# Optimization experiments

Hardware: AMD Instinct MI355X
Metric: run time of the kernel (lower is better)

## Reference

```python
import jax, jax.numpy as jnp
import numpy as np

B, T, K = 128, 2048, 96  # batch, seq_len, num_tags


def setup_inputs() -> dict:
    key = jax.random.key(0)
    k1, k2, k3, k4, k5 = jax.random.split(key, 5)
    logits = jax.random.normal(k1, (B, T, K), dtype=jnp.float32)
    labels = jax.random.randint(k2, (B, T), 0, K)
    mask = jnp.ones((B, T), dtype=bool)
    # learned CRF parameters
    transitions = jax.random.normal(k3, (K, K), dtype=jnp.float32) * 0.1
    start_transitions = jax.random.normal(k4, (K,), dtype=jnp.float32) * 0.1
    end_transitions = jax.random.normal(k5, (K,), dtype=jnp.float32) * 0.1
    return {
        "logits": logits,
        "labels": labels,
        "mask": mask,
        "transitions": transitions,
        "start_transitions": start_transitions,
        "end_transitions": end_transitions,
    }


def _log_partition(logits, maskf, transitions, start_transitions, end_transitions):
    # forward algorithm over time via scan; logits: [B,T,K]
    em = jnp.transpose(logits, (1, 0, 2))   # [T,B,K]
    mk = jnp.transpose(maskf, (1, 0))       # [T,B]
    alpha0 = start_transitions[None, :] + em[0]  # [B,K]

    def step(alpha, x):
        emit_t, m_t = x
        # alpha[b,i] + transitions[i,j] + emit[b,j] -> logsumexp over i
        inner = alpha[:, :, None] + transitions[None, :, :] + emit_t[:, None, :]
        new = jax.nn.logsumexp(inner, axis=1)
        alpha = jnp.where(m_t[:, None] > 0, new, alpha)
        return alpha, None

    alpha, _ = jax.lax.scan(step, alpha0, (em[1:], mk[1:]))
    return jax.nn.logsumexp(alpha + end_transitions[None, :], axis=1)  # [B]


def _joint_score(logits, labels, maskf, mask, transitions, start_transitions, end_transitions):
    b = jnp.arange(logits.shape[0])
    emit = jnp.take_along_axis(logits, labels[..., None], axis=2)[..., 0]  # [B,T]
    emit_sum = jnp.sum(emit * maskf, axis=1)
    trans = transitions[labels[:, :-1], labels[:, 1:]]                     # [B,T-1]
    trans_sum = jnp.sum(trans * maskf[:, 1:], axis=1)
    seq_len = jnp.sum(mask.astype(jnp.int32), axis=1)
    last_tags = labels[b, seq_len - 1]
    return start_transitions[labels[:, 0]] + emit_sum + trans_sum + end_transitions[last_tags]


def reference(logits, labels, mask, transitions, start_transitions, end_transitions):
    maskf = mask.astype(logits.dtype)
    logZ = _log_partition(logits, maskf, transitions, start_transitions, end_transitions)
    score = _joint_score(logits, labels, maskf, mask, transitions, start_transitions, end_transitions)
    log_lik = jnp.sum(score - logZ)
    return -log_lik
```

## Files before the change

### kernel.cpp

```cpp
#include <hip/hip_runtime.h>
#include <math.h>

#define B_ 128
#define T_ 2048
#define K_ 96
#define NC 256
#define CH 8
#define WARM 8
#define GRP 16
#define SP 100
#define LOGZ_BLOCKS (8 * NC)
#define SCORE_BLOCKS 512

typedef __attribute__((ext_vector_type(8))) short short8;
typedef __attribute__((ext_vector_type(4))) float float4v;
union U8 { unsigned u[4]; short8 v; };

__device__ __forceinline__ unsigned pack_trunc(float lo, float hi) {
    return __builtin_amdgcn_perm(__builtin_bit_cast(unsigned, hi),
                                 __builtin_bit_cast(unsigned, lo), 0x07060302u);
}
__device__ __forceinline__ unsigned short bf16_rne(float x) {
    unsigned u = __builtin_bit_cast(unsigned, x);
    u += 0x7FFFu + ((u >> 16) & 1u);
    return (unsigned short)(u >> 16);
}
__device__ __forceinline__ float wave_reduce_sum(float x) {
#pragma unroll
    for (int off = 1; off < 64; off <<= 1) x += __shfl_xor(x, off, 64);
    return x;
}

__device__ __forceinline__ void crf_mfma_step(
    int k, int len, float* __restrict__ Sw, int lo, int q,
    const short8 (&Bf)[6][3], const float* (&ep)[4],
    float (&e)[24], float &acc)
{
#pragma unroll
    for (int i = 0; i < 24; ++i) e[i] = __expf(e[i]);

    float bn0 = Sw[lo * SP];
    float R = __builtin_amdgcn_rcpf(bn0);
    acc += __logf(bn0);

    short8 Af[3];
#pragma unroll
    for (int f = 0; f < 3; ++f) {
        const float4* pp = (const float4*)&Sw[lo * SP + 32 * f + 8 * q];
        float4 v0 = pp[0], v1 = pp[1];
        U8 ua;
        ua.u[0] = pack_trunc(v0.x * R, v0.y * R);
        ua.u[1] = pack_trunc(v0.z * R, v0.w * R);
        ua.u[2] = pack_trunc(v1.x * R, v1.y * R);
        ua.u[3] = pack_trunc(v1.z * R, v1.w * R);
        Af[f] = ua.v;
    }

    float4v Cv[6];
#pragma unroll
    for (int nt = 0; nt < 6; ++nt) {
        float4v cz = {0.f, 0.f, 0.f, 0.f};
        cz = __builtin_amdgcn_mfma_f32_16x16x32_bf16(Af[0], Bf[nt][0], cz, 0, 0, 0);
        cz = __builtin_amdgcn_mfma_f32_16x16x32_bf16(Af[1], Bf[nt][1], cz, 0, 0, 0);
        Cv[nt] = __builtin_amdgcn_mfma_f32_16x16x32_bf16(Af[2], Bf[nt][2], cz, 0, 0, 0);
    }

#pragma unroll
    for (int nt = 0; nt < 6; ++nt)
#pragma unroll
        for (int r = 0; r < 4; ++r)
            Sw[(4 * q + r) * SP + 16 * nt + lo] = Cv[nt][r] * e[nt * 4 + r];

    if (k + 2 <= len) {
#pragma unroll
        for (int r = 0; r < 4; ++r) {
#pragma unroll
            for (int nt = 0; nt < 6; ++nt) e[nt * 4 + r] = ep[r][16 * nt];
            ep[r] += K_;
        }
    }
}

__global__ void __launch_bounds__(64, 3) crf_fused_kernel(
    const float* __restrict__ logits, const int* __restrict__ labels,
    const float* __restrict__ trans, const float* __restrict__ startT,
    const float* __restrict__ endT, float* __restrict__ out)
{
    __shared__ __align__(16) float Sw[GRP * SP];
    const int tid = threadIdx.x;

    if (blockIdx.x >= LOGZ_BLOCKS) {
        int gid = (blockIdx.x - LOGZ_BLOCKS) * 64 + tid;
        float acc2 = 0.f;
        for (int i = gid; i < B_ * T_; i += SCORE_BLOCKS * 64) {
            int b = i >> 11, t = i & (T_ - 1);
            const int* lab = labels + (size_t)b * T_;
            int lt = lab[t];
            acc2 += logits[((size_t)b * T_ + t) * K_ + lt];
            acc2 += (t > 0) ? trans[lab[t - 1] * K_ + lt] : startT[lt];
            if (t == T_ - 1) acc2 += endT[lt];
        }
        acc2 = wave_reduce_sum(acc2);
        if (tid == 0) atomicAdd(out, -acc2);
        return;
    }

    const int lane = tid, lo = lane & 15, q = lane >> 4;
    const int W = blockIdx.x;
    const int c = W & (NC - 1);
    const int grp = W >> 8;
    const int ts = (c == 0) ? 0 : (CH * c - WARM);
    const int len = (c == 0) ? CH : ((c < NC - 1) ? (WARM + CH) : (WARM + CH - 1));

    short8 Bf[6][3];
#pragma unroll
    for (int nt = 0; nt < 6; ++nt)
#pragma unroll
        for (int kf = 0; kf < 3; ++kf) {
            U8 ub;
#pragma unroll
            for (int p = 0; p < 4; ++p) {
                int k0 = 32 * kf + 8 * q + 2 * p;
                int n = 16 * nt + lo;
                unsigned l = bf16_rne(__expf(trans[(size_t)k0 * K_ + n]));
                unsigned h = bf16_rne(__expf(trans[(size_t)(k0 + 1) * K_ + n]));
                ub.u[p] = l | (h << 16);
            }
            Bf[nt][kf] = ub.v;
        }

    if (c == 0) {
#pragma unroll
        for (int f = 0; f < 3; ++f) {
            int k0 = 32 * f + 8 * q;
            const float* p = logits + (size_t)(grp * GRP + lo) * T_ * K_ + k0;
            float4 La = *(const float4*)p, Lb2 = *(const float4*)(p + 4);
            float4 Sa = *(const float4*)(startT + k0), Sb = *(const float4*)(startT + k0 + 4);
            float4 w0 = { __expf(La.x + Sa.x), __expf(La.y + Sa.y),
                          __expf(La.z + Sa.z), __expf(La.w + Sa.w) };
            float4 w1 = { __expf(Lb2.x + Sb.x), __expf(Lb2.y + Sb.y),
                          __expf(Lb2.z + Sb.z), __expf(Lb2.w + Sb.w) };
            float4* d0 = (float4*)&Sw[lo * SP + k0];
            d0[0] = w0; d0[1] = w1;
        }
    } else {
        float4 one = {1.f, 1.f, 1.f, 1.f};
#pragma unroll
        for (int f = 0; f < 3; ++f) {
            float4* d0 = (float4*)&Sw[lo * SP + 32 * f + 8 * q];
            d0[0] = one; d0[1] = one;
        }
    }

    const float* ep[4];
#pragma unroll
    for (int r = 0; r < 4; ++r)
        ep[r] = logits + ((size_t)(grp * GRP + 4 * q + r) * T_ + (ts + 1)) * K_ + lo;
    float eO[24], eE[24];
#pragma unroll
    for (int r = 0; r < 4; ++r) {
#pragma unroll
        for (int nt = 0; nt < 6; ++nt) eO[nt * 4 + r] = ep[r][16 * nt];
        ep[r] += K_;
    }
#pragma unroll
    for (int r = 0; r < 4; ++r) {
#pragma unroll
        for (int nt = 0; nt < 6; ++nt) eE[nt * 4 + r] = ep[r][16 * nt];
        ep[r] += K_;
    }

    float acc = 0.f, Mwarm = 0.f;
    int k = 1;
    if (c != 0) {
#pragma unroll 1
        for (int n2 = 0; n2 < WARM / 2; ++n2) {
            crf_mfma_step(k, len, Sw, lo, q, Bf, ep, eO, acc); ++k;
            crf_mfma_step(k, len, Sw, lo, q, Bf, ep, eE, acc); ++k;
        }
        float mx = 0.f;
#pragma unroll
        for (int f = 0; f < 3; ++f) {
            const float4* pp = (const float4*)&Sw[lo * SP + 32 * f + 8 * q];
            float4 v0 = pp[0], v1 = pp[1];
            mx = fmaxf(mx, fmaxf(fmaxf(v0.x, v0.y), fmaxf(v0.z, v0.w)));
            mx = fmaxf(mx, fmaxf(fmaxf(v1.x, v1.y), fmaxf(v1.z, v1.w)));
        }
        mx = fmaxf(mx, __shfl_xor(mx, 16, 64));
        mx = fmaxf(mx, __shfl_xor(mx, 32, 64));
        Mwarm = __logf(mx) + acc;
    }

    const int pairs = (len - k + 1) >> 1;
#pragma unroll 1
    for (int n2 = 0; n2 < pairs; ++n2) {
        crf_mfma_step(k, len, Sw, lo, q, Bf, ep, eO, acc); ++k;
        crf_mfma_step(k, len, Sw, lo, q, Bf, ep, eE, acc); ++k;
    }
    if (k <= len) { crf_mfma_step(k, len, Sw, lo, q, Bf, ep, eO, acc); ++k; }

    float contrib;
    if (c < NC - 1) {
        float mx = 0.f;
#pragma unroll
        for (int f = 0; f < 3; ++f) {
            const float4* pp = (const float4*)&Sw[lo * SP + 32 * f + 8 * q];
            float4 v0 = pp[0], v1 = pp[1];
            mx = fmaxf(mx, fmaxf(fmaxf(v0.x, v0.y), fmaxf(v0.z, v0.w)));
            mx = fmaxf(mx, fmaxf(fmaxf(v1.x, v1.y), fmaxf(v1.z, v1.w)));
        }
        mx = fmaxf(mx, __shfl_xor(mx, 16, 64));
        mx = fmaxf(mx, __shfl_xor(mx, 32, 64));
        contrib = __logf(mx) + acc - Mwarm;
    } else {
        float xs[24];
#pragma unroll
        for (int f = 0; f < 3; ++f) {
            int k0 = 32 * f + 8 * q;
            const float4* pp = (const float4*)&Sw[lo * SP + k0];
            float4 v0 = pp[0], v1 = pp[1];
            float4 e0 = *(const float4*)(endT + k0), e1 = *(const float4*)(endT + k0 + 4);
            xs[f * 8 + 0] = __logf(v0.x) + e0.x; xs[f * 8 + 1] = __logf(v0.y) + e0.y;
            xs[f * 8 + 2] = __logf(v0.z) + e0.z; xs[f * 8 + 3] = __logf(v0.w) + e0.w;
            xs[f * 8 + 4] = __logf(v1.x) + e1.x; xs[f * 8 + 5] = __logf(v1.y) + e1.y;
            xs[f * 8 + 6] = __logf(v1.z) + e1.z; xs[f * 8 + 7] = __logf(v1.w) + e1.w;
        }
        float m2 = -1e30f;
#pragma unroll
        for (int i = 0; i < 24; ++i) m2 = fmaxf(m2, xs[i]);
        m2 = fmaxf(m2, __shfl_xor(m2, 16, 64));
        m2 = fmaxf(m2, __shfl_xor(m2, 32, 64));
        float p2 = 0.f;
#pragma unroll
        for (int i = 0; i < 24; ++i) p2 += __expf(xs[i] - m2);
        p2 += __shfl_xor(p2, 16, 64);
        p2 += __shfl_xor(p2, 32, 64);
        contrib = m2 + __logf(p2) + acc - Mwarm;
    }

    float cv = (lane < 16) ? contrib : 0.f;
    cv = wave_reduce_sum(cv);
    if (lane == 0) atomicAdd(out, cv);
}

extern "C" void kernel_launch(void* const* d_in, const int* in_sizes, int n_in,
                              void* d_out, int out_size, void* d_ws, size_t ws_size,
                              hipStream_t stream)
{
    const float* logits = (const float*)d_in[0];
    const int*   labels = (const int*)d_in[1];
    const float* trans  = (const float*)d_in[3];
    const float* startT = (const float*)d_in[4];
    const float* endT   = (const float*)d_in[5];
    float* out = (float*)d_out;

    hipMemsetAsync(out, 0, sizeof(float), stream);
    hipLaunchKernelGGL(crf_fused_kernel, dim3(LOGZ_BLOCKS + SCORE_BLOCKS),
                       dim3(64), 0, stream,
                       logits, labels, trans, startT, endT, out);
}
```

Measured before the change: 197.7 us.

## Restructure CRF step with vectorized emission loads and fewer, longer chunks

Changes the chunked forward recurrence so that each step multiplies the emission into the A operand, using exp(emit) applied to the previous state held in registers, instead of into the stored output. Emission loads become contiguous float4 reads per lane in place of strided scalar loads. Normalization now uses a lane-0 shuffle of the MFMA result rather than an LDS read. Chunk count is halved and chunk length doubled, which shrinks the warm-up overhead fraction but halves the parallelism, and the occupancy hint drops from 3 to 2 waves.

```diff
diff --git a/kernel.cpp b/kernel.cpp
--- a/kernel.cpp
+++ b/kernel.cpp
@@ -4,13 +4,13 @@
 #define B_ 128
 #define T_ 2048
 #define K_ 96
-#define NC 256
-#define CH 8
+#define NC 128
+#define CH 16
 #define WARM 8
 #define GRP 16
 #define SP 100
 #define LOGZ_BLOCKS (8 * NC)
-#define SCORE_BLOCKS 512
+#define SCORE_BLOCKS 256
 
 typedef __attribute__((ext_vector_type(8))) short short8;
 typedef __attribute__((ext_vector_type(4))) float float4v;
@@ -31,29 +31,39 @@
     return x;
 }
 
-__device__ __forceinline__ void crf_mfma_step(
+__device__ __forceinline__ void crf_step(
     int k, int len, float* __restrict__ Sw, int lo, int q,
-    const short8 (&Bf)[6][3], const float* (&ep)[4],
-    float (&e)[24], float &acc)
+    const short8 (&Bf)[6][3], const float* __restrict__ eptr,
+    float4 (&eb)[6], float4 (&cvN)[6], float &acc)
 {
-#pragma unroll
-    for (int i = 0; i < 24; ++i) e[i] = __expf(e[i]);
-
-    float bn0 = Sw[lo * SP];
-    float R = __builtin_amdgcn_rcpf(bn0);
-    acc += __logf(bn0);
+    float4 pr[6];
+#pragma unroll
+    for (int i = 0; i < 6; ++i) {
+        float4 e = eb[i], cc = cvN[i];
+        pr[i] = make_float4(cc.x * __expf(e.x), cc.y * __expf(e.y),
+                            cc.z * __expf(e.z), cc.w * __expf(e.w));
+    }
 
     short8 Af[3];
 #pragma unroll
     for (int f = 0; f < 3; ++f) {
-        const float4* pp = (const float4*)&Sw[lo * SP + 32 * f + 8 * q];
-        float4 v0 = pp[0], v1 = pp[1];
+        float4 v0 = pr[2 * f], v1 = pr[2 * f + 1];
         U8 ua;
-        ua.u[0] = pack_trunc(v0.x * R, v0.y * R);
-        ua.u[1] = pack_trunc(v0.z * R, v0.w * R);
-        ua.u[2] = pack_trunc(v1.x * R, v1.y * R);
-        ua.u[3] = pack_trunc(v1.z * R, v1.w * R);
+        ua.u[0] = pack_trunc(v0.x, v0.y);
+        ua.u[1] = pack_trunc(v0.z, v0.w);
+        ua.u[2] = pack_trunc(v1.x, v1.y);
+        ua.u[3] = pack_trunc(v1.z, v1.w);
         Af[f] = ua.v;
+    }
+
+    if (k + 2 <= len) {
+        const float* p = eptr + (size_t)(k + 1) * K_;
+        eb[0] = *(const float4*)(p);
+        eb[1] = *(const float4*)(p + 4);
+        eb[2] = *(const float4*)(p + 32);
+        eb[3] = *(const float4*)(p + 36);
+        eb[4] = *(const float4*)(p + 64);
+        eb[5] = *(const float4*)(p + 68);
     }
 
     float4v Cv[6];
@@ -65,23 +75,36 @@
         Cv[nt] = __builtin_amdgcn_mfma_f32_16x16x32_bf16(Af[2], Bf[nt][2], cz, 0, 0, 0);
     }
 
+    float c00 = __shfl(Cv[0][0], 0, 64);
+    float R = __builtin_amdgcn_rcpf(c00);
+    acc += __logf(c00);
+
 #pragma unroll
     for (int nt = 0; nt < 6; ++nt)
 #pragma unroll
         for (int r = 0; r < 4; ++r)
-            Sw[(4 * q + r) * SP + 16 * nt + lo] = Cv[nt][r] * e[nt * 4 + r];
-
-    if (k + 2 <= len) {
-#pragma unroll
-        for (int r = 0; r < 4; ++r) {
-#pragma unroll
-            for (int nt = 0; nt < 6; ++nt) e[nt * 4 + r] = ep[r][16 * nt];
-            ep[r] += K_;
-        }
-    }
-}
-
-__global__ void __launch_bounds__(64, 3) crf_fused_kernel(
+            Sw[(4 * q + r) * SP + 16 * nt + lo] = Cv[nt][r] * R;
+
+#pragma unroll
+    for (int f = 0; f < 3; ++f) {
+        cvN[2 * f]     = *(const float4*)&Sw[lo * SP + 32 * f + 8 * q];
+        cvN[2 * f + 1] = *(const float4*)&Sw[lo * SP + 32 * f + 8 * q + 4];
+    }
+}
+
+__device__ __forceinline__ float measureM(const float4 (&cvN)[6], float acc) {
+    float mx = 0.f;
+#pragma unroll
+    for (int i = 0; i < 6; ++i) {
+        float4 v = cvN[i];
+        mx = fmaxf(mx, fmaxf(fmaxf(v.x, v.y), fmaxf(v.z, v.w)));
+    }
+    mx = fmaxf(mx, __shfl_xor(mx, 16, 64));
+    mx = fmaxf(mx, __shfl_xor(mx, 32, 64));
+    return __logf(mx) + acc;
+}
+
+__global__ void __launch_bounds__(64, 2) crf_fused_kernel(
     const float* __restrict__ logits, const int* __restrict__ labels,
     const float* __restrict__ trans, const float* __restrict__ startT,
     const float* __restrict__ endT, float* __restrict__ out)
@@ -108,7 +131,7 @@
     const int lane = tid, lo = lane & 15, q = lane >> 4;
     const int W = blockIdx.x;
     const int c = W & (NC - 1);
-    const int grp = W >> 8;
+    const int grp = W >> 7;
     const int ts = (c == 0) ? 0 : (CH * c - WARM);
     const int len = (c == 0) ? CH : ((c < NC - 1) ? (WARM + CH) : (WARM + CH - 1));
 
@@ -129,45 +152,33 @@
             Bf[nt][kf] = ub.v;
         }
 
+    float4 cvN[6];
     if (c == 0) {
 #pragma unroll
         for (int f = 0; f < 3; ++f) {
             int k0 = 32 * f + 8 * q;
-            const float* p = logits + (size_t)(grp * GRP + lo) * T_ * K_ + k0;
-            float4 La = *(const float4*)p, Lb2 = *(const float4*)(p + 4);
-            float4 Sa = *(const float4*)(startT + k0), Sb = *(const float4*)(startT + k0 + 4);
-            float4 w0 = { __expf(La.x + Sa.x), __expf(La.y + Sa.y),
-                          __expf(La.z + Sa.z), __expf(La.w + Sa.w) };
-            float4 w1 = { __expf(Lb2.x + Sb.x), __expf(Lb2.y + Sb.y),
-                          __expf(Lb2.z + Sb.z), __expf(Lb2.w + Sb.w) };
-            float4* d0 = (float4*)&Sw[lo * SP + k0];
-            d0[0] = w0; d0[1] = w1;
+            float4 s0 = *(const float4*)(startT + k0);
+            float4 s1 = *(const float4*)(startT + k0 + 4);
+            cvN[2 * f]     = make_float4(__expf(s0.x), __expf(s0.y), __expf(s0.z), __expf(s0.w));
+            cvN[2 * f + 1] = make_float4(__expf(s1.x), __expf(s1.y), __expf(s1.z), __expf(s1.w));
         }
     } else {
-        float4 one = {1.f, 1.f, 1.f, 1.f};
-#pragma unroll
-        for (int f = 0; f < 3; ++f) {
-            float4* d0 = (float4*)&Sw[lo * SP + 32 * f + 8 * q];
-            d0[0] = one; d0[1] = one;
-        }
-    }
-
-    const float* ep[4];
-#pragma unroll
-    for (int r = 0; r < 4; ++r)
-        ep[r] = logits + ((size_t)(grp * GRP + 4 * q + r) * T_ + (ts + 1)) * K_ + lo;
-    float eO[24], eE[24];
-#pragma unroll
-    for (int r = 0; r < 4; ++r) {
-#pragma unroll
-        for (int nt = 0; nt < 6; ++nt) eO[nt * 4 + r] = ep[r][16 * nt];
-        ep[r] += K_;
-    }
-#pragma unroll
-    for (int r = 0; r < 4; ++r) {
-#pragma unroll
-        for (int nt = 0; nt < 6; ++nt) eE[nt * 4 + r] = ep[r][16 * nt];
-        ep[r] += K_;
+        float4 one = make_float4(1.f, 1.f, 1.f, 1.f);
+#pragma unroll
+        for (int i = 0; i < 6; ++i) cvN[i] = one;
+    }
+
+    const float* eptr = logits + ((size_t)(grp * GRP + lo) * T_ + ts) * K_ + 8 * q;
+    float4 eb0[6], eb1[6];
+    {
+        const float* p0 = eptr;
+        eb0[0] = *(const float4*)(p0);      eb0[1] = *(const float4*)(p0 + 4);
+        eb0[2] = *(const float4*)(p0 + 32); eb0[3] = *(const float4*)(p0 + 36);
+        eb0[4] = *(const float4*)(p0 + 64); eb0[5] = *(const float4*)(p0 + 68);
+        const float* p1 = eptr + K_;
+        eb1[0] = *(const float4*)(p1);      eb1[1] = *(const float4*)(p1 + 4);
+        eb1[2] = *(const float4*)(p1 + 32); eb1[3] = *(const float4*)(p1 + 36);
+        eb1[4] = *(const float4*)(p1 + 64); eb1[5] = *(const float4*)(p1 + 68);
     }
 
     float acc = 0.f, Mwarm = 0.f;
@@ -175,72 +186,59 @@
     if (c != 0) {
 #pragma unroll 1
         for (int n2 = 0; n2 < WARM / 2; ++n2) {
-            crf_mfma_step(k, len, Sw, lo, q, Bf, ep, eO, acc); ++k;
-            crf_mfma_step(k, len, Sw, lo, q, Bf, ep, eE, acc); ++k;
-        }
-        float mx = 0.f;
-#pragma unroll
-        for (int f = 0; f < 3; ++f) {
-            const float4* pp = (const float4*)&Sw[lo * SP + 32 * f + 8 * q];
-            float4 v0 = pp[0], v1 = pp[1];
-            mx = fmaxf(mx, fmaxf(fmaxf(v0.x, v0.y), fmaxf(v0.z, v0.w)));
-            mx = fmaxf(mx, fmaxf(fmaxf(v1.x, v1.y), fmaxf(v1.z, v1.w)));
-        }
-        mx = fmaxf(mx, __shfl_xor(mx, 16, 64));
-        mx = fmaxf(mx, __shfl_xor(mx, 32, 64));
-        Mwarm = __logf(mx) + acc;
+            crf_step(k, len, Sw, lo, q, Bf, eptr, eb0, cvN, acc); ++k;
+            crf_step(k, len, Sw, lo, q, Bf, eptr, eb1, cvN, acc); ++k;
+        }
+        Mwarm = measureM(cvN, acc);
     }
 
     const int pairs = (len - k + 1) >> 1;
 #pragma unroll 1
     for (int n2 = 0; n2 < pairs; ++n2) {
-        crf_mfma_step(k, len, Sw, lo, q, Bf, ep, eO, acc); ++k;
-        crf_mfma_step(k, len, Sw, lo, q, Bf, ep, eE, acc); ++k;
-    }
-    if (k <= len) { crf_mfma_step(k, len, Sw, lo, q, Bf, ep, eO, acc); ++k; }
+        crf_step(k, len, Sw, lo, q, Bf, eptr, eb0, cvN, acc); ++k;
+        crf_step(k, len, Sw, lo, q, Bf, eptr, eb1, cvN, acc); ++k;
+    }
+    if (k <= len) { crf_step(k, len, Sw, lo, q, Bf, eptr, eb0, cvN, acc); ++k; }
 
     float contrib;
     if (c < NC - 1) {
-        float mx = 0.f;
-#pragma unroll
-        for (int f = 0; f < 3; ++f) {
-            const float4* pp = (const float4*)&Sw[lo * SP + 32 * f + 8 * q];
-            float4 v0 = pp[0], v1 = pp[1];
-            mx = fmaxf(mx, fmaxf(fmaxf(v0.x, v0.y), fmaxf(v0.z, v0.w)));
-            mx = fmaxf(mx, fmaxf(fmaxf(v1.x, v1.y), fmaxf(v1.z, v1.w)));
-        }
-        mx = fmaxf(mx, __shfl_xor(mx, 16, 64));
-        mx = fmaxf(mx, __shfl_xor(mx, 32, 64));
-        contrib = __logf(mx) + acc - Mwarm;
+        contrib = measureM(cvN, acc) - Mwarm;
     } else {
-        float xs[24];
+        const float* pe = eptr + (size_t)len * K_;
+        float xv[24];
 #pragma unroll
         for (int f = 0; f < 3; ++f) {
             int k0 = 32 * f + 8 * q;
-            const float4* pp = (const float4*)&Sw[lo * SP + k0];
-            float4 v0 = pp[0], v1 = pp[1];
-            float4 e0 = *(const float4*)(endT + k0), e1 = *(const float4*)(endT + k0 + 4);
-            xs[f * 8 + 0] = __logf(v0.x) + e0.x; xs[f * 8 + 1] = __logf(v0.y) + e0.y;
-            xs[f * 8 + 2] = __logf(v0.z) + e0.z; xs[f * 8 + 3] = __logf(v0.w) + e0.w;
-            xs[f * 8 + 4] = __logf(v1.x) + e1.x; xs[f * 8 + 5] = __logf(v1.y) + e1.y;
-            xs[f * 8 + 6] = __logf(v1.z) + e1.z; xs[f * 8 + 7] = __logf(v1.w) + e1.w;
+            float4 e0 = *(const float4*)(pe + 32 * f);
+            float4 e1 = *(const float4*)(pe + 32 * f + 4);
+            float4 d0 = *(const float4*)(endT + k0);
+            float4 d1 = *(const float4*)(endT + k0 + 4);
+            float4 c0 = cvN[2 * f], c1 = cvN[2 * f + 1];
+            xv[f * 8 + 0] = __logf(c0.x) + e0.x + d0.x;
+            xv[f * 8 + 1] = __logf(c0.y) + e0.y + d0.y;
+            xv[f * 8 + 2] = __logf(c0.z) + e0.z + d0.z;
+            xv[f * 8 + 3] = __logf(c0.w) + e0.w + d0.w;
+            xv[f * 8 + 4] = __logf(c1.x) + e1.x + d1.x;
+            xv[f * 8 + 5] = __logf(c1.y) + e1.y + d1.y;
+            xv[f * 8 + 6] = __logf(c1.z) + e1.z + d1.z;
+            xv[f * 8 + 7] = __logf(c1.w) + e1.w + d1.w;
         }
         float m2 = -1e30f;
 #pragma unroll
-        for (int i = 0; i < 24; ++i) m2 = fmaxf(m2, xs[i]);
+        for (int i = 0; i < 24; ++i) m2 = fmaxf(m2, xv[i]);
         m2 = fmaxf(m2, __shfl_xor(m2, 16, 64));
         m2 = fmaxf(m2, __shfl_xor(m2, 32, 64));
         float p2 = 0.f;
 #pragma unroll
-        for (int i = 0; i < 24; ++i) p2 += __expf(xs[i] - m2);
+        for (int i = 0; i < 24; ++i) p2 += __expf(xv[i] - m2);
         p2 += __shfl_xor(p2, 16, 64);
         p2 += __shfl_xor(p2, 32, 64);
         contrib = m2 + __logf(p2) + acc - Mwarm;
     }
 
-    float cv = (lane < 16) ? contrib : 0.f;
-    cv = wave_reduce_sum(cv);
-    if (lane == 0) atomicAdd(out, cv);
+    float cvv = (lane < 16) ? contrib : 0.f;
+    cvv = wave_reduce_sum(cvv);
+    if (lane == 0) atomicAdd(out, cvv);
 }
 
 extern "C" void kernel_launch(void* const* d_in, const int* in_sizes, int n_in,
```

After: 187.0 us. -5.4%, faster.
